# Kernel optimization log

Hardware: AMD Instinct MI355X
Metric: run time of the kernel (lower is better)

Reference implementation:

```python
import jax, jax.numpy as jnp
import numpy as np

N = 100000
E = 1600000
F_IN, F_HID, F_OUT = 128, 32, 2


def setup_inputs() -> dict:
    key = jax.random.key(0)
    k1, k2, k3, k4 = jax.random.split(key, 4)
    x = jax.random.normal(k1, (N, F_IN), dtype=jnp.float32)
    edge_index = jax.random.randint(k2, (2, E), 0, N, dtype=jnp.int64)
    # Glorot-style init like torch_geometric GCNConv
    W1 = jax.random.normal(k3, (F_IN, F_HID), dtype=jnp.float32) * (1.0 / np.sqrt(F_IN))
    b1 = jnp.zeros((F_HID,), dtype=jnp.float32)
    W2 = jax.random.normal(k4, (F_HID, F_OUT), dtype=jnp.float32) * (1.0 / np.sqrt(F_HID))
    b2 = jnp.zeros((F_OUT,), dtype=jnp.float32)
    return {"x": x, "edge_index": edge_index, "W1": W1, "b1": b1, "W2": W2, "b2": b2}


def _gcn_conv(x, row, col, norm, W, b):
    # GCNConv: transform, then normalized aggregate (source -> target), then bias
    h = x @ W                                   # [N, F_out]
    msg = norm[:, None] * h[row]                # gather + scale, [E+N, F_out]
    out = jax.ops.segment_sum(msg, col, num_segments=N)  # scatter-add to targets
    return out + b


def reference(x, edge_index, W1, b1, W2, b2):
    # add self-loops (GCNConv default)
    loops = jnp.arange(N, dtype=edge_index.dtype)
    row = jnp.concatenate([edge_index[0], loops])
    col = jnp.concatenate([edge_index[1], loops])
    # symmetric normalization: deg^{-1/2}[row] * deg^{-1/2}[col], deg = in-degree w/ self-loops
    deg = jax.ops.segment_sum(jnp.ones_like(col, dtype=x.dtype), col, num_segments=N)
    dinv = jnp.where(deg > 0, jax.lax.rsqrt(deg), 0.0)
    norm = dinv[row] * dinv[col]                # [E+N]

    h = _gcn_conv(x, row, col, norm, W1, b1)
    h = jax.nn.relu(h)
    h = _gcn_conv(h, row, col, norm, W2, b2)
    return jax.nn.log_softmax(h, axis=1)
```

## Files before the change

### kernel.cpp

```cpp
#include <hip/hip_runtime.h>
#include <hip/hip_bf16.h>
#include <math.h>
#include <stdint.h>


#define GNN_N 100000
#define GNN_E 1600000
#define NBUCK 782
#define CAP 2560
#define CHB 4096
#define EB 391
#define XPAD 136

typedef float fx2 __attribute__((ext_vector_type(2)));
typedef short short8x __attribute__((ext_vector_type(8)));
typedef float f32x4 __attribute__((ext_vector_type(4)));

__device__ inline uint16_t bf16_bits(float f) {
    uint32_t u = __float_as_uint(f);
    return (uint16_t)((u + 0x7fffu + ((u >> 16) & 1u)) >> 16);
}
__device__ inline uint32_t pack_bf2(float lo, float hi) {
    return (uint32_t)bf16_bits(lo) | ((uint32_t)bf16_bits(hi) << 16);
}

__global__ __launch_bounds__(256) void k_fat(const int* __restrict__ row,
                                             const int* __restrict__ col,
                                             int* __restrict__ bucket_fill,
                                             uint32_t* __restrict__ slab,
                                             const float* __restrict__ x,
                                             const float* __restrict__ W1,
                                             uint32_t* __restrict__ h1,
                                             int e, int n) {
    __shared__ union {
        struct { int hist[NBUCK]; int base[NBUCK]; } bk;
        struct { uint16_t xs[64 * XPAD]; uint16_t w1t[32 * XPAD]; } mm;
    } u;
    const int tid = threadIdx.x;

    if (blockIdx.x < EB) {
        int* hist = u.bk.hist;
        int* base = u.bk.base;
        const int e0 = blockIdx.x * CHB;
        const int m = min(CHB, e - e0);
        const bool full = (m == CHB);

        for (int i = tid; i < NBUCK; i += 256) hist[i] = 0;

        int cc[16], rr[16], pp[16];
        if (full) {
            const int4* c4 = (const int4*)(col + e0);
            const int4* r4 = (const int4*)(row + e0);
            #pragma unroll
            for (int t = 0; t < 4; ++t) {
                int4 c = c4[tid + t * 256];
                int4 r = r4[tid + t * 256];
                cc[t * 4 + 0] = c.x; cc[t * 4 + 1] = c.y;
                cc[t * 4 + 2] = c.z; cc[t * 4 + 3] = c.w;
                rr[t * 4 + 0] = r.x; rr[t * 4 + 1] = r.y;
                rr[t * 4 + 2] = r.z; rr[t * 4 + 3] = r.w;
            }
            __syncthreads();
            #pragma unroll
            for (int t = 0; t < 16; ++t)
                pp[t] = atomicAdd(&hist[cc[t] >> 7], 1);
        } else {
            __syncthreads();
            #pragma unroll
            for (int t = 0; t < 16; ++t) {
                int i = tid + t * 256;
                if (i < m) {
                    cc[t] = col[e0 + i];
                    rr[t] = row[e0 + i];
                    pp[t] = atomicAdd(&hist[cc[t] >> 7], 1);
                }
            }
        }
        __syncthreads();
        for (int i = tid; i < NBUCK; i += 256) {
            int bb = (i + blockIdx.x * 131) % NBUCK;
            base[bb] = atomicAdd(&bucket_fill[bb], hist[bb]);
        }
        __syncthreads();
        if (full) {
            #pragma unroll
            for (int t = 0; t < 16; ++t) {
                int b = cc[t] >> 7;
                int p = base[b] + pp[t];
                if (p < CAP)
                    slab[(size_t)b * CAP + p] = ((uint32_t)rr[t] << 7) | (uint32_t)(cc[t] & 127);
            }
        } else {
            #pragma unroll
            for (int t = 0; t < 16; ++t) {
                int i = tid + t * 256;
                if (i < m) {
                    int b = cc[t] >> 7;
                    int p = base[b] + pp[t];
                    if (p < CAP)
                        slab[(size_t)b * CAP + p] = ((uint32_t)rr[t] << 7) | (uint32_t)(cc[t] & 127);
                }
            }
        }
    } else {
        uint16_t* xs = u.mm.xs;
        uint16_t* w1t = u.mm.w1t;
        const int nodeBase = (blockIdx.x - EB) * 64;

        for (int i = tid; i < 4096; i += 256) {
            int k = i >> 5, c = i & 31;
            w1t[c * XPAD + k] = bf16_bits(W1[i]);
        }
        {
            const float4* x4 = (const float4*)x;
            for (int i = tid; i < 64 * 32; i += 256) {
                int node = i >> 5;
                int k4 = i & 31;
                float4 v = make_float4(0.f, 0.f, 0.f, 0.f);
                if (nodeBase + node < n)
                    v = x4[(size_t)(nodeBase + node) * 32 + k4];
                int b = node * XPAD + k4 * 4;
                xs[b + 0] = bf16_bits(v.x); xs[b + 1] = bf16_bits(v.y);
                xs[b + 2] = bf16_bits(v.z); xs[b + 3] = bf16_bits(v.w);
            }
        }
        __syncthreads();

        const int wave = tid >> 6;
        const int lane = tid & 63;
        const int nn = lane & 15;
        const int quad = lane >> 4;
        f32x4 acc0 = {0.f, 0.f, 0.f, 0.f};
        f32x4 acc1 = {0.f, 0.f, 0.f, 0.f};
        const int xrow = (wave * 16 + nn) * XPAD;
        #pragma unroll
        for (int s = 0; s < 4; ++s) {
            const int kof = s * 32 + quad * 8;
            short8x bfrag = *(const short8x*)&xs[xrow + kof];
            short8x a0 = *(const short8x*)&w1t[nn * XPAD + kof];
            short8x a1 = *(const short8x*)&w1t[(16 + nn) * XPAD + kof];
            acc0 = __builtin_amdgcn_mfma_f32_16x16x32_bf16(a0, bfrag, acc0, 0, 0, 0);
            acc1 = __builtin_amdgcn_mfma_f32_16x16x32_bf16(a1, bfrag, acc1, 0, 0, 0);
        }
        const int gn = nodeBase + wave * 16 + nn;
        if (gn < n) {
            uint2* h1b2 = (uint2*)h1;
            h1b2[(size_t)gn * 8 + quad] =
                make_uint2(pack_bf2(acc0[0], acc0[1]), pack_bf2(acc0[2], acc0[3]));
            h1b2[(size_t)gn * 8 + 4 + quad] =
                make_uint2(pack_bf2(acc1[0], acc1[1]), pack_bf2(acc1[2], acc1[3]));
        }
    }
}

__global__ __launch_bounds__(512) void k_fine(uint32_t* __restrict__ slab,
                                              const int* __restrict__ bucket_fill,
                                              uint32_t* __restrict__ h1,
                                              uint32_t* __restrict__ offsets,
                                              float* __restrict__ dinv, int n) {
    __shared__ int hist[128];
    __shared__ int excl[128];
    __shared__ int wsum[2];
    __shared__ uint32_t stage[CAP];
    const int tid = threadIdx.x;
    const int b = blockIdx.x;
    const int lane = tid & 63, wave = tid >> 6;

    if (tid < 128) hist[tid] = 0;
    __syncthreads();
    const int nb = min(bucket_fill[b], CAP);
    uint32_t* sl = slab + (size_t)b * CAP;

    uint32_t uu[5];
    int pp[5];
    #pragma unroll
    for (int j = 0; j < 5; ++j) {
        int i = tid + j * 512;
        if (i < nb) {
            uint32_t u = sl[i];
            uu[j] = u;
            pp[j] = atomicAdd(&hist[u & 127u], 1);
        }
    }
    __syncthreads();
    int v = 0, inc = 0;
    if (tid < 128) {
        v = hist[tid];
        inc = v;
        #pragma unroll
        for (int d = 1; d < 64; d <<= 1) {
            int t = __shfl_up(inc, d);
            if (lane >= d) inc += t;
        }
        if (lane == 63) wsum[wave] = inc;
    }
    __syncthreads();
    if (tid == 0) { int t0 = wsum[0]; wsum[0] = 0; wsum[1] = t0; }
    __syncthreads();
    if (tid < 128) {
        int ex = inc - v + wsum[wave];
        excl[tid] = ex;
        int c = b * 128 + tid;
        if (c < n) {
            offsets[c] = ((uint32_t)min(v, 2047) << 21) | (uint32_t)(b * CAP + ex);
            dinv[c] = rsqrtf((float)(v + 1));
        }
    }
    __syncthreads();
    #pragma unroll
    for (int j = 0; j < 5; ++j) {
        int i = tid + j * 512;
        if (i < nb)
            stage[excl[uu[j] & 127u] + pp[j]] = uu[j] >> 7;
    }
    const uint2* h1b2 = (const uint2*)h1;
    uint2 ru[2]; float rdc[2]; int rc[2], rq[2]; bool rvld[2];
    #pragma unroll
    for (int it = 0; it < 2; ++it) {
        int d = tid + it * 512;
        int node = d >> 3;
        rq[it] = d & 7;
        int c = b * 128 + node;
        rc[it] = c;
        rvld[it] = (c < n);
        if (rvld[it]) {
            rdc[it] = rsqrtf((float)(hist[node] + 1));
            ru[it] = h1b2[(size_t)c * 8 + rq[it]];
        }
    }
    __syncthreads();
    #pragma unroll
    for (int it = 0; it < 2; ++it) {
        if (rvld[it]) {
            float dc = rdc[it];
            uint2 u2 = ru[it];
            float a0 = __uint_as_float(u2.x << 16) * dc;
            float a1 = __uint_as_float(u2.x & 0xffff0000u) * dc;
            float a2 = __uint_as_float(u2.y << 16) * dc;
            float a3 = __uint_as_float(u2.y & 0xffff0000u) * dc;
            int w = 0;
            w = __builtin_amdgcn_cvt_pk_fp8_f32(a0, a1, w, false);
            w = __builtin_amdgcn_cvt_pk_fp8_f32(a2, a3, w, true);
            h1[(size_t)rc[it] * 16 + rq[it]] = (uint32_t)w;
        }
    }
    for (int i = tid; i < nb; i += 512)
        sl[i] = stage[i];
}

__device__ inline void fp8x16_acc(float* a, uint4 u) {
    fx2 p;
    p = __builtin_amdgcn_cvt_pk_f32_fp8(u.x, false); a[0] += p.x;  a[1] += p.y;
    p = __builtin_amdgcn_cvt_pk_f32_fp8(u.x, true);  a[2] += p.x;  a[3] += p.y;
    p = __builtin_amdgcn_cvt_pk_f32_fp8(u.y, false); a[4] += p.x;  a[5] += p.y;
    p = __builtin_amdgcn_cvt_pk_f32_fp8(u.y, true);  a[6] += p.x;  a[7] += p.y;
    p = __builtin_amdgcn_cvt_pk_f32_fp8(u.z, false); a[8] += p.x;  a[9] += p.y;
    p = __builtin_amdgcn_cvt_pk_f32_fp8(u.z, true);  a[10] += p.x; a[11] += p.y;
    p = __builtin_amdgcn_cvt_pk_f32_fp8(u.w, false); a[12] += p.x; a[13] += p.y;
    p = __builtin_amdgcn_cvt_pk_f32_fp8(u.w, true);  a[14] += p.x; a[15] += p.y;
}

__global__ __launch_bounds__(256) void k_gather1(const uint32_t* __restrict__ offsets,
                                                 const uint32_t* __restrict__ sorted,
                                                 const uint32_t* __restrict__ h1,
                                                 const float* __restrict__ dinv,
                                                 const float* __restrict__ b1,
                                                 const float* __restrict__ W2,
                                                 float* __restrict__ h2s, int n) {
    __shared__ float sb1[32];
    __shared__ float sW2[64];
    const int tid = threadIdx.x;
    if (tid < 32) sb1[tid] = b1[tid];
    else if (tid < 96) sW2[tid - 32] = W2[tid - 32];
    __syncthreads();

    const int l = tid & 1;
    const int node = blockIdx.x * 128 + (tid >> 1);
    if (node >= n) return;
    const uint4* h4 = (const uint4*)h1;
    float acc[16], acc2[16];
    #pragma unroll
    for (int j = 0; j < 16; ++j) { acc[j] = 0.f; acc2[j] = 0.f; }
    fp8x16_acc(acc, h4[(size_t)node * 4 + l]);
    const uint32_t ow = offsets[node];
    const int start = (int)(ow & 0x1FFFFFu);
    const int deg = (int)(ow >> 21);
    const uint32_t* sr = sorted + start;
    int k = 0;
    for (; k + 8 <= deg; k += 8) {
        int r[8];
        uint4 u[8];
        #pragma unroll
        for (int t = 0; t < 8; ++t) r[t] = (int)sr[k + t];
        #pragma unroll
        for (int t = 0; t < 8; ++t) u[t] = h4[(size_t)r[t] * 4 + l];
        #pragma unroll
        for (int t = 0; t < 8; ++t) fp8x16_acc((t & 1) ? acc2 : acc, u[t]);
    }
    for (; k + 2 <= deg; k += 2) {
        int ra = (int)sr[k], rb = (int)sr[k + 1];
        uint4 ua = h4[(size_t)ra * 4 + l];
        uint4 ub = h4[(size_t)rb * 4 + l];
        fp8x16_acc(acc, ua);
        fp8x16_acc(acc2, ub);
    }
    if (k < deg)
        fp8x16_acc(acc, h4[(size_t)sr[k] * 4 + l]);
    #pragma unroll
    for (int j = 0; j < 16; ++j) acc[j] += acc2[j];

    const float dc = dinv[node];
    const int f0 = l * 16;
    float s0 = 0.f, s1 = 0.f;
    #pragma unroll
    for (int j = 0; j < 16; ++j) {
        float a = fmaxf(dc * acc[j] + sb1[f0 + j], 0.f);
        s0 += a * sW2[(f0 + j) * 2];
        s1 += a * sW2[(f0 + j) * 2 + 1];
    }
    s0 += __shfl_xor(s0, 1);
    s1 += __shfl_xor(s1, 1);
    if (l == 0) ((float2*)h2s)[node] = make_float2(dc * s0, dc * s1);
}

__global__ __launch_bounds__(256) void k_gather2(const uint32_t* __restrict__ offsets,
                                                 const uint32_t* __restrict__ sorted,
                                                 const float* __restrict__ h2s,
                                                 const float* __restrict__ dinv,
                                                 const float* __restrict__ b2,
                                                 float* __restrict__ out, int n) {
    const int tid = threadIdx.x;
    const int l = tid & 3;
    const int node = blockIdx.x * 64 + (tid >> 2);
    if (node >= n) return;
    const float2* h2 = (const float2*)h2s;
    float sx = 0.f, sy = 0.f;
    if (l == 0) { float2 s = h2[node]; sx = s.x; sy = s.y; }
    const uint32_t ow = offsets[node];
    const int start = (int)(ow & 0x1FFFFFu);
    const int deg = (int)(ow >> 21);
    for (int k = l; k < deg; k += 4) {
        float2 v = h2[sorted[start + k]];
        sx += v.x; sy += v.y;
    }
    sx += __shfl_xor(sx, 1); sx += __shfl_xor(sx, 2);
    sy += __shfl_xor(sy, 1); sy += __shfl_xor(sy, 2);
    if (l == 0) {
        float d = dinv[node];
        float v0 = d * sx + b2[0];
        float v1 = d * sy + b2[1];
        float m = fmaxf(v0, v1);
        float lg = m + logf(expf(v0 - m) + expf(v1 - m));
        ((float2*)out)[node] = make_float2(v0 - lg, v1 - lg);
    }
}

extern "C" void kernel_launch(void* const* d_in, const int* in_sizes, int n_in,
                              void* d_out, int out_size, void* d_ws, size_t ws_size,
                              hipStream_t stream) {
    const float* x  = (const float*)d_in[0];
    const int*   ei = (const int*)d_in[1];
    const float* W1 = (const float*)d_in[2];
    const float* b1 = (const float*)d_in[3];
    const float* W2 = (const float*)d_in[4];
    const float* b2 = (const float*)d_in[5];
    float* out = (float*)d_out;
    char* ws = (char*)d_ws;

    const int N = GNN_N, E = GNN_E;
    const int* row = ei;
    const int* col = ei + GNN_E;

    float*    dinv        = (float*)    ws;
    uint32_t* offsets     = (uint32_t*)(ws + 4ull *  100000);
    int*      bucket_fill = (int*)     (ws + 4ull *  200000);
    float*    h2s         = (float*)   (ws + 4ull *  201024);
    uint32_t* h1          = (uint32_t*)(ws + 4ull *  401024);
    uint32_t* slab        = (uint32_t*)(ws + 4ull * 2001024);

    hipMemsetAsync(bucket_fill, 0, 1024 * sizeof(int), stream);

    const int MB = (N + 63) / 64;
    k_fat    <<<EB + MB, 256, 0, stream>>>(row, col, bucket_fill, slab, x, W1, h1, E, N);
    k_fine   <<<NBUCK, 512, 0, stream>>>(slab, bucket_fill, h1, offsets, dinv, N);
    k_gather1<<<(N + 127) / 128, 256, 0, stream>>>(offsets, slab, h1, dinv, b1, W2, h2s, N);
    k_gather2<<<(N + 63) / 64, 256, 0, stream>>>(offsets, slab, h2s, dinv, b2, out, N);
}
```

Measured before the change: 171.4 us.

## Write unscaled FP8 h1 directly from GEMM and apply source dinv in gather

The GEMM now quantizes h1 straight to FP8 instead of writing bf16, so k_fine no longer reads bf16 h1, scales it by dinv and rewrites it as FP8. The per-source normalization moves into the first gather, which loads dinv[row] per edge and fuses it as a multiply-add. This removes a full read and rewrite of h1 and shrinks the workspace. In exchange the gather issues one extra scattered 4-byte load per edge, and FP8 now quantizes the unscaled values, which changes the rounding error.

```diff
diff --git a/kernel.cpp b/kernel.cpp
--- a/kernel.cpp
+++ b/kernel.cpp
@@ -20,9 +20,6 @@
     uint32_t u = __float_as_uint(f);
     return (uint16_t)((u + 0x7fffu + ((u >> 16) & 1u)) >> 16);
 }
-__device__ inline uint32_t pack_bf2(float lo, float hi) {
-    return (uint32_t)bf16_bits(lo) | ((uint32_t)bf16_bits(hi) << 16);
-}
 
 __global__ __launch_bounds__(256) void k_fat(const int* __restrict__ row,
                                              const int* __restrict__ col,
@@ -30,7 +27,7 @@
                                              uint32_t* __restrict__ slab,
                                              const float* __restrict__ x,
                                              const float* __restrict__ W1,
-                                             uint32_t* __restrict__ h1,
+                                             uint32_t* __restrict__ h1q,
                                              int e, int n) {
     __shared__ union {
         struct { int hist[NBUCK]; int base[NBUCK]; } bk;
@@ -144,18 +141,19 @@
         }
         const int gn = nodeBase + wave * 16 + nn;
         if (gn < n) {
-            uint2* h1b2 = (uint2*)h1;
-            h1b2[(size_t)gn * 8 + quad] =
-                make_uint2(pack_bf2(acc0[0], acc0[1]), pack_bf2(acc0[2], acc0[3]));
-            h1b2[(size_t)gn * 8 + 4 + quad] =
-                make_uint2(pack_bf2(acc1[0], acc1[1]), pack_bf2(acc1[2], acc1[3]));
+            int w0 = 0, w1 = 0;
+            w0 = __builtin_amdgcn_cvt_pk_fp8_f32(acc0[0], acc0[1], w0, false);
+            w0 = __builtin_amdgcn_cvt_pk_fp8_f32(acc0[2], acc0[3], w0, true);
+            w1 = __builtin_amdgcn_cvt_pk_fp8_f32(acc1[0], acc1[1], w1, false);
+            w1 = __builtin_amdgcn_cvt_pk_fp8_f32(acc1[2], acc1[3], w1, true);
+            h1q[(size_t)gn * 8 + quad] = (uint32_t)w0;
+            h1q[(size_t)gn * 8 + 4 + quad] = (uint32_t)w1;
         }
     }
 }
 
 __global__ __launch_bounds__(512) void k_fine(uint32_t* __restrict__ slab,
                                               const int* __restrict__ bucket_fill,
-                                              uint32_t* __restrict__ h1,
                                               uint32_t* __restrict__ offsets,
                                               float* __restrict__ dinv, int n) {
     __shared__ int hist[128];
@@ -213,56 +211,26 @@
         if (i < nb)
             stage[excl[uu[j] & 127u] + pp[j]] = uu[j] >> 7;
     }
-    const uint2* h1b2 = (const uint2*)h1;
-    uint2 ru[2]; float rdc[2]; int rc[2], rq[2]; bool rvld[2];
-    #pragma unroll
-    for (int it = 0; it < 2; ++it) {
-        int d = tid + it * 512;
-        int node = d >> 3;
-        rq[it] = d & 7;
-        int c = b * 128 + node;
-        rc[it] = c;
-        rvld[it] = (c < n);
-        if (rvld[it]) {
-            rdc[it] = rsqrtf((float)(hist[node] + 1));
-            ru[it] = h1b2[(size_t)c * 8 + rq[it]];
-        }
-    }
-    __syncthreads();
-    #pragma unroll
-    for (int it = 0; it < 2; ++it) {
-        if (rvld[it]) {
-            float dc = rdc[it];
-            uint2 u2 = ru[it];
-            float a0 = __uint_as_float(u2.x << 16) * dc;
-            float a1 = __uint_as_float(u2.x & 0xffff0000u) * dc;
-            float a2 = __uint_as_float(u2.y << 16) * dc;
-            float a3 = __uint_as_float(u2.y & 0xffff0000u) * dc;
-            int w = 0;
-            w = __builtin_amdgcn_cvt_pk_fp8_f32(a0, a1, w, false);
-            w = __builtin_amdgcn_cvt_pk_fp8_f32(a2, a3, w, true);
-            h1[(size_t)rc[it] * 16 + rq[it]] = (uint32_t)w;
-        }
-    }
+    __syncthreads();
     for (int i = tid; i < nb; i += 512)
         sl[i] = stage[i];
 }
 
-__device__ inline void fp8x16_acc(float* a, uint4 u) {
+__device__ inline void fp8x16_fma(float* a, uint4 u, float s) {
     fx2 p;
-    p = __builtin_amdgcn_cvt_pk_f32_fp8(u.x, false); a[0] += p.x;  a[1] += p.y;
-    p = __builtin_amdgcn_cvt_pk_f32_fp8(u.x, true);  a[2] += p.x;  a[3] += p.y;
-    p = __builtin_amdgcn_cvt_pk_f32_fp8(u.y, false); a[4] += p.x;  a[5] += p.y;
-    p = __builtin_amdgcn_cvt_pk_f32_fp8(u.y, true);  a[6] += p.x;  a[7] += p.y;
-    p = __builtin_amdgcn_cvt_pk_f32_fp8(u.z, false); a[8] += p.x;  a[9] += p.y;
-    p = __builtin_amdgcn_cvt_pk_f32_fp8(u.z, true);  a[10] += p.x; a[11] += p.y;
-    p = __builtin_amdgcn_cvt_pk_f32_fp8(u.w, false); a[12] += p.x; a[13] += p.y;
-    p = __builtin_amdgcn_cvt_pk_f32_fp8(u.w, true);  a[14] += p.x; a[15] += p.y;
+    p = __builtin_amdgcn_cvt_pk_f32_fp8(u.x, false); a[0] += s * p.x;  a[1] += s * p.y;
+    p = __builtin_amdgcn_cvt_pk_f32_fp8(u.x, true);  a[2] += s * p.x;  a[3] += s * p.y;
+    p = __builtin_amdgcn_cvt_pk_f32_fp8(u.y, false); a[4] += s * p.x;  a[5] += s * p.y;
+    p = __builtin_amdgcn_cvt_pk_f32_fp8(u.y, true);  a[6] += s * p.x;  a[7] += s * p.y;
+    p = __builtin_amdgcn_cvt_pk_f32_fp8(u.z, false); a[8] += s * p.x;  a[9] += s * p.y;
+    p = __builtin_amdgcn_cvt_pk_f32_fp8(u.z, true);  a[10] += s * p.x; a[11] += s * p.y;
+    p = __builtin_amdgcn_cvt_pk_f32_fp8(u.w, false); a[12] += s * p.x; a[13] += s * p.y;
+    p = __builtin_amdgcn_cvt_pk_f32_fp8(u.w, true);  a[14] += s * p.x; a[15] += s * p.y;
 }
 
 __global__ __launch_bounds__(256) void k_gather1(const uint32_t* __restrict__ offsets,
                                                  const uint32_t* __restrict__ sorted,
-                                                 const uint32_t* __restrict__ h1,
+                                                 const uint32_t* __restrict__ h1q,
                                                  const float* __restrict__ dinv,
                                                  const float* __restrict__ b1,
                                                  const float* __restrict__ W2,
@@ -277,11 +245,12 @@
     const int l = tid & 1;
     const int node = blockIdx.x * 128 + (tid >> 1);
     if (node >= n) return;
-    const uint4* h4 = (const uint4*)h1;
+    const uint4* h4 = (const uint4*)h1q;
+    const float dc = dinv[node];
     float acc[16], acc2[16];
     #pragma unroll
     for (int j = 0; j < 16; ++j) { acc[j] = 0.f; acc2[j] = 0.f; }
-    fp8x16_acc(acc, h4[(size_t)node * 4 + l]);
+    fp8x16_fma(acc, h4[(size_t)node * 2 + l], dc);
     const uint32_t ow = offsets[node];
     const int start = (int)(ow & 0x1FFFFFu);
     const int deg = (int)(ow >> 21);
@@ -289,27 +258,30 @@
     int k = 0;
     for (; k + 8 <= deg; k += 8) {
         int r[8];
+        float dv[8];
         uint4 u[8];
         #pragma unroll
         for (int t = 0; t < 8; ++t) r[t] = (int)sr[k + t];
         #pragma unroll
-        for (int t = 0; t < 8; ++t) u[t] = h4[(size_t)r[t] * 4 + l];
-        #pragma unroll
-        for (int t = 0; t < 8; ++t) fp8x16_acc((t & 1) ? acc2 : acc, u[t]);
+        for (int t = 0; t < 8; ++t) { dv[t] = dinv[r[t]]; u[t] = h4[(size_t)r[t] * 2 + l]; }
+        #pragma unroll
+        for (int t = 0; t < 8; ++t) fp8x16_fma((t & 1) ? acc2 : acc, u[t], dv[t]);
     }
     for (; k + 2 <= deg; k += 2) {
         int ra = (int)sr[k], rb = (int)sr[k + 1];
-        uint4 ua = h4[(size_t)ra * 4 + l];
-        uint4 ub = h4[(size_t)rb * 4 + l];
-        fp8x16_acc(acc, ua);
-        fp8x16_acc(acc2, ub);
-    }
-    if (k < deg)
-        fp8x16_acc(acc, h4[(size_t)sr[k] * 4 + l]);
+        float da = dinv[ra], db = dinv[rb];
+        uint4 ua = h4[(size_t)ra * 2 + l];
+        uint4 ub = h4[(size_t)rb * 2 + l];
+        fp8x16_fma(acc, ua, da);
+        fp8x16_fma(acc2, ub, db);
+    }
+    if (k < deg) {
+        int ra = (int)sr[k];
+        fp8x16_fma(acc, h4[(size_t)ra * 2 + l], dinv[ra]);
+    }
     #pragma unroll
     for (int j = 0; j < 16; ++j) acc[j] += acc2[j];
 
-    const float dc = dinv[node];
     const int f0 = l * 16;
     float s0 = 0.f, s1 = 0.f;
     #pragma unroll
@@ -375,14 +347,14 @@
     uint32_t* offsets     = (uint32_t*)(ws + 4ull *  100000);
     int*      bucket_fill = (int*)     (ws + 4ull *  200000);
     float*    h2s         = (float*)   (ws + 4ull *  201024);
-    uint32_t* h1          = (uint32_t*)(ws + 4ull *  401024);
-    uint32_t* slab        = (uint32_t*)(ws + 4ull * 2001024);
+    uint32_t* h1q         = (uint32_t*)(ws + 4ull *  401024);
+    uint32_t* slab        = (uint32_t*)(ws + 4ull * 1201024);
 
     hipMemsetAsync(bucket_fill, 0, 1024 * sizeof(int), stream);
 
     const int MB = (N + 63) / 64;
-    k_fat    <<<EB + MB, 256, 0, stream>>>(row, col, bucket_fill, slab, x, W1, h1, E, N);
-    k_fine   <<<NBUCK, 512, 0, stream>>>(slab, bucket_fill, h1, offsets, dinv, N);
-    k_gather1<<<(N + 127) / 128, 256, 0, stream>>>(offsets, slab, h1, dinv, b1, W2, h2s, N);
+    k_fat    <<<EB + MB, 256, 0, stream>>>(row, col, bucket_fill, slab, x, W1, h1q, E, N);
+    k_fine   <<<NBUCK, 512, 0, stream>>>(slab, bucket_fill, offsets, dinv, N);
+    k_gather1<<<(N + 127) / 128, 256, 0, stream>>>(offsets, slab, h1q, dinv, b1, W2, h2s, N);
     k_gather2<<<(N + 63) / 64, 256, 0, stream>>>(offsets, slab, h2s, dinv, b2, out, N);
 }
```

Result: no change. 172.2 us (+0.4%).

## Widen destination buckets to 256 nodes and compact the fp8 h1 buffer

Applied to the files above, without the earlier changes.

Edge bucketing now groups destination nodes in buckets of 256 instead of 128. That halves the number of buckets, raises slab capacity, and packs 8 local bits instead of 7. The fp8 copy of h1 is now written by k_fine to a separate, densely packed buffer with a 32-byte stride per node, instead of in place inside the 64-byte-stride bf16 buffer. The random gathers in k_gather1 therefore touch half the memory footprint and get better cache-line use. The trade-off is fewer, larger k_fine blocks, with more register arrays and a bigger shared stage per block, which lowers parallelism in that kernel.

```diff
diff --git a/kernel.cpp b/kernel.cpp
--- a/kernel.cpp
+++ b/kernel.cpp
@@ -6,8 +6,8 @@
 
 #define GNN_N 100000
 #define GNN_E 1600000
-#define NBUCK 782
-#define CAP 2560
+#define NBUCK 391
+#define CAP 4608
 #define CHB 4096
 #define EB 391
 #define XPAD 136
@@ -30,7 +30,7 @@
                                              uint32_t* __restrict__ slab,
                                              const float* __restrict__ x,
                                              const float* __restrict__ W1,
-                                             uint32_t* __restrict__ h1,
+                                             uint32_t* __restrict__ h1b,
                                              int e, int n) {
     __shared__ union {
         struct { int hist[NBUCK]; int base[NBUCK]; } bk;
@@ -63,7 +63,7 @@
             __syncthreads();
             #pragma unroll
             for (int t = 0; t < 16; ++t)
-                pp[t] = atomicAdd(&hist[cc[t] >> 7], 1);
+                pp[t] = atomicAdd(&hist[cc[t] >> 8], 1);
         } else {
             __syncthreads();
             #pragma unroll
@@ -72,7 +72,7 @@
                 if (i < m) {
                     cc[t] = col[e0 + i];
                     rr[t] = row[e0 + i];
-                    pp[t] = atomicAdd(&hist[cc[t] >> 7], 1);
+                    pp[t] = atomicAdd(&hist[cc[t] >> 8], 1);
                 }
             }
         }
@@ -85,20 +85,20 @@
         if (full) {
             #pragma unroll
             for (int t = 0; t < 16; ++t) {
-                int b = cc[t] >> 7;
+                int b = cc[t] >> 8;
                 int p = base[b] + pp[t];
                 if (p < CAP)
-                    slab[(size_t)b * CAP + p] = ((uint32_t)rr[t] << 7) | (uint32_t)(cc[t] & 127);
+                    slab[(size_t)b * CAP + p] = ((uint32_t)rr[t] << 8) | (uint32_t)(cc[t] & 255);
             }
         } else {
             #pragma unroll
             for (int t = 0; t < 16; ++t) {
                 int i = tid + t * 256;
                 if (i < m) {
-                    int b = cc[t] >> 7;
+                    int b = cc[t] >> 8;
                     int p = base[b] + pp[t];
                     if (p < CAP)
-                        slab[(size_t)b * CAP + p] = ((uint32_t)rr[t] << 7) | (uint32_t)(cc[t] & 127);
+                        slab[(size_t)b * CAP + p] = ((uint32_t)rr[t] << 8) | (uint32_t)(cc[t] & 255);
                 }
             }
         }
@@ -144,7 +144,7 @@
         }
         const int gn = nodeBase + wave * 16 + nn;
         if (gn < n) {
-            uint2* h1b2 = (uint2*)h1;
+            uint2* h1b2 = (uint2*)h1b;
             h1b2[(size_t)gn * 8 + quad] =
                 make_uint2(pack_bf2(acc0[0], acc0[1]), pack_bf2(acc0[2], acc0[3]));
             h1b2[(size_t)gn * 8 + 4 + quad] =
@@ -155,36 +155,37 @@
 
 __global__ __launch_bounds__(512) void k_fine(uint32_t* __restrict__ slab,
                                               const int* __restrict__ bucket_fill,
-                                              uint32_t* __restrict__ h1,
+                                              const uint32_t* __restrict__ h1b,
+                                              uint16_t* __restrict__ h1q16,
                                               uint32_t* __restrict__ offsets,
                                               float* __restrict__ dinv, int n) {
-    __shared__ int hist[128];
-    __shared__ int excl[128];
-    __shared__ int wsum[2];
+    __shared__ int hist[256];
+    __shared__ int excl[256];
+    __shared__ int wsum[4];
     __shared__ uint32_t stage[CAP];
     const int tid = threadIdx.x;
     const int b = blockIdx.x;
     const int lane = tid & 63, wave = tid >> 6;
 
-    if (tid < 128) hist[tid] = 0;
+    if (tid < 256) hist[tid] = 0;
     __syncthreads();
     const int nb = min(bucket_fill[b], CAP);
     uint32_t* sl = slab + (size_t)b * CAP;
 
-    uint32_t uu[5];
-    int pp[5];
-    #pragma unroll
-    for (int j = 0; j < 5; ++j) {
+    uint32_t uu[9];
+    int pp[9];
+    #pragma unroll
+    for (int j = 0; j < 9; ++j) {
         int i = tid + j * 512;
         if (i < nb) {
             uint32_t u = sl[i];
             uu[j] = u;
-            pp[j] = atomicAdd(&hist[u & 127u], 1);
+            pp[j] = atomicAdd(&hist[u & 255u], 1);
         }
     }
     __syncthreads();
     int v = 0, inc = 0;
-    if (tid < 128) {
+    if (tid < 256) {
         v = hist[tid];
         inc = v;
         #pragma unroll
@@ -195,12 +196,16 @@
         if (lane == 63) wsum[wave] = inc;
     }
     __syncthreads();
-    if (tid == 0) { int t0 = wsum[0]; wsum[0] = 0; wsum[1] = t0; }
-    __syncthreads();
-    if (tid < 128) {
+    if (tid == 0) {
+        int a = 0;
+        #pragma unroll
+        for (int w = 0; w < 4; ++w) { int t = wsum[w]; wsum[w] = a; a += t; }
+    }
+    __syncthreads();
+    if (tid < 256) {
         int ex = inc - v + wsum[wave];
         excl[tid] = ex;
-        int c = b * 128 + tid;
+        int c = b * 256 + tid;
         if (c < n) {
             offsets[c] = ((uint32_t)min(v, 2047) << 21) | (uint32_t)(b * CAP + ex);
             dinv[c] = rsqrtf((float)(v + 1));
@@ -208,42 +213,26 @@
     }
     __syncthreads();
     #pragma unroll
-    for (int j = 0; j < 5; ++j) {
+    for (int j = 0; j < 9; ++j) {
         int i = tid + j * 512;
         if (i < nb)
-            stage[excl[uu[j] & 127u] + pp[j]] = uu[j] >> 7;
-    }
-    const uint2* h1b2 = (const uint2*)h1;
-    uint2 ru[2]; float rdc[2]; int rc[2], rq[2]; bool rvld[2];
-    #pragma unroll
-    for (int it = 0; it < 2; ++it) {
-        int d = tid + it * 512;
-        int node = d >> 3;
-        rq[it] = d & 7;
-        int c = b * 128 + node;
-        rc[it] = c;
-        rvld[it] = (c < n);
-        if (rvld[it]) {
-            rdc[it] = rsqrtf((float)(hist[node] + 1));
-            ru[it] = h1b2[(size_t)c * 8 + rq[it]];
-        }
-    }
-    __syncthreads();
-    #pragma unroll
-    for (int it = 0; it < 2; ++it) {
-        if (rvld[it]) {
-            float dc = rdc[it];
-            uint2 u2 = ru[it];
-            float a0 = __uint_as_float(u2.x << 16) * dc;
-            float a1 = __uint_as_float(u2.x & 0xffff0000u) * dc;
-            float a2 = __uint_as_float(u2.y << 16) * dc;
-            float a3 = __uint_as_float(u2.y & 0xffff0000u) * dc;
-            int w = 0;
-            w = __builtin_amdgcn_cvt_pk_fp8_f32(a0, a1, w, false);
-            w = __builtin_amdgcn_cvt_pk_fp8_f32(a2, a3, w, true);
-            h1[(size_t)rc[it] * 16 + rq[it]] = (uint32_t)w;
-        }
-    }
+            stage[excl[uu[j] & 255u] + pp[j]] = uu[j] >> 8;
+    }
+    #pragma unroll
+    for (int it = 0; it < 8; ++it) {
+        int i = tid + it * 512;
+        int node = i >> 4, j = i & 15;
+        int c = b * 256 + node;
+        if (c < n) {
+            float dc = rsqrtf((float)(hist[node] + 1));
+            uint32_t w = h1b[(size_t)c * 16 + j];
+            float lo = __uint_as_float(w << 16) * dc;
+            float hi = __uint_as_float(w & 0xffff0000u) * dc;
+            int pk = __builtin_amdgcn_cvt_pk_fp8_f32(lo, hi, 0, false);
+            h1q16[(size_t)c * 16 + j] = (uint16_t)pk;
+        }
+    }
+    __syncthreads();
     for (int i = tid; i < nb; i += 512)
         sl[i] = stage[i];
 }
@@ -262,7 +251,7 @@
 
 __global__ __launch_bounds__(256) void k_gather1(const uint32_t* __restrict__ offsets,
                                                  const uint32_t* __restrict__ sorted,
-                                                 const uint32_t* __restrict__ h1,
+                                                 const uint32_t* __restrict__ h1q,
                                                  const float* __restrict__ dinv,
                                                  const float* __restrict__ b1,
                                                  const float* __restrict__ W2,
@@ -277,11 +266,11 @@
     const int l = tid & 1;
     const int node = blockIdx.x * 128 + (tid >> 1);
     if (node >= n) return;
-    const uint4* h4 = (const uint4*)h1;
+    const uint4* h4 = (const uint4*)h1q;
     float acc[16], acc2[16];
     #pragma unroll
     for (int j = 0; j < 16; ++j) { acc[j] = 0.f; acc2[j] = 0.f; }
-    fp8x16_acc(acc, h4[(size_t)node * 4 + l]);
+    fp8x16_acc(acc, h4[(size_t)node * 2 + l]);
     const uint32_t ow = offsets[node];
     const int start = (int)(ow & 0x1FFFFFu);
     const int deg = (int)(ow >> 21);
@@ -293,19 +282,19 @@
         #pragma unroll
         for (int t = 0; t < 8; ++t) r[t] = (int)sr[k + t];
         #pragma unroll
-        for (int t = 0; t < 8; ++t) u[t] = h4[(size_t)r[t] * 4 + l];
+        for (int t = 0; t < 8; ++t) u[t] = h4[(size_t)r[t] * 2 + l];
         #pragma unroll
         for (int t = 0; t < 8; ++t) fp8x16_acc((t & 1) ? acc2 : acc, u[t]);
     }
     for (; k + 2 <= deg; k += 2) {
         int ra = (int)sr[k], rb = (int)sr[k + 1];
-        uint4 ua = h4[(size_t)ra * 4 + l];
-        uint4 ub = h4[(size_t)rb * 4 + l];
+        uint4 ua = h4[(size_t)ra * 2 + l];
+        uint4 ub = h4[(size_t)rb * 2 + l];
         fp8x16_acc(acc, ua);
         fp8x16_acc(acc2, ub);
     }
     if (k < deg)
-        fp8x16_acc(acc, h4[(size_t)sr[k] * 4 + l]);
+        fp8x16_acc(acc, h4[(size_t)(int)sr[k] * 2 + l]);
     #pragma unroll
     for (int j = 0; j < 16; ++j) acc[j] += acc2[j];
 
@@ -375,14 +364,16 @@
     uint32_t* offsets     = (uint32_t*)(ws + 4ull *  100000);
     int*      bucket_fill = (int*)     (ws + 4ull *  200000);
     float*    h2s         = (float*)   (ws + 4ull *  201024);
-    uint32_t* h1          = (uint32_t*)(ws + 4ull *  401024);
-    uint32_t* slab        = (uint32_t*)(ws + 4ull * 2001024);
+    uint32_t* h1q         = (uint32_t*)(ws + 4ull *  401024);
+    uint32_t* h1b         = (uint32_t*)(ws + 4ull * 1201024);
+    uint32_t* slab        = (uint32_t*)(ws + 4ull * 2801024);
 
     hipMemsetAsync(bucket_fill, 0, 1024 * sizeof(int), stream);
 
     const int MB = (N + 63) / 64;
-    k_fat    <<<EB + MB, 256, 0, stream>>>(row, col, bucket_fill, slab, x, W1, h1, E, N);
-    k_fine   <<<NBUCK, 512, 0, stream>>>(slab, bucket_fill, h1, offsets, dinv, N);
-    k_gather1<<<(N + 127) / 128, 256, 0, stream>>>(offsets, slab, h1, dinv, b1, W2, h2s, N);
+    k_fat    <<<EB + MB, 256, 0, stream>>>(row, col, bucket_fill, slab, x, W1, h1b, E, N);
+    k_fine   <<<NBUCK, 512, 0, stream>>>(slab, bucket_fill, h1b, (uint16_t*)h1q,
+                                         offsets, dinv, N);
+    k_gather1<<<(N + 127) / 128, 256, 0, stream>>>(offsets, slab, h1q, dinv, b1, W2, h2s, N);
     k_gather2<<<(N + 63) / 64, 256, 0, stream>>>(offsets, slab, h2s, dinv, b2, out, N);
 }
```

New measurement: 166.3 us. -3.0%, faster.
